# Optimization experiments

Hardware: AMD Instinct MI355X
Metric: run time of the kernel (lower is better)

The kernel has to match this reference:

```python
import jax, jax.numpy as jnp
import numpy as np

SEQ_LEN, N_FEAT, EMB = 512, 8, 64
HID = 2 * EMB  # 128
BATCH = 512


def _lstm_layer(x, Wih, Whh, bih, bhh):
    """Single-layer LSTM, batch_first x: [B,T,F]. PyTorch gate order i,f,g,o.
    Returns (outputs [B,T,H], final hidden [B,H])."""
    B = x.shape[0]
    H = Whh.shape[1]
    # precompute input projections for all timesteps: [B,T,4H]
    xp = jnp.einsum('btf,gf->btg', x, Wih) + bih + bhh

    def step(carry, xt):
        h, c = carry
        gates = xt + h @ Whh.T  # [B,4H]
        i, f, g, o = jnp.split(gates, 4, axis=-1)
        i = jax.nn.sigmoid(i)
        f = jax.nn.sigmoid(f)
        g = jnp.tanh(g)
        o = jax.nn.sigmoid(o)
        c = f * c + i * g
        h = o * jnp.tanh(c)
        return (h, c), h

    h0 = jnp.zeros((B, H), dtype=x.dtype)
    c0 = jnp.zeros((B, H), dtype=x.dtype)
    (hT, _), hs = jax.lax.scan(step, (h0, c0), xp.transpose(1, 0, 2))
    return hs.transpose(1, 0, 2), hT


def setup_inputs() -> dict:
    key = jax.random.key(0)
    ks = jax.random.split(key, 13)
    inp = {"x": jax.random.normal(ks[0], (BATCH, SEQ_LEN, N_FEAT), dtype=jnp.float32)}

    def mk(k, shape, fan):
        s = 1.0 / np.sqrt(fan)
        return jax.random.uniform(k, shape, dtype=jnp.float32, minval=-s, maxval=s)

    # layer 1: in=N_FEAT, hid=HID
    inp["Wih1"] = mk(ks[1], (4 * HID, N_FEAT), HID)
    inp["Whh1"] = mk(ks[2], (4 * HID, HID), HID)
    inp["bih1"] = mk(ks[3], (4 * HID,), HID)
    inp["bhh1"] = mk(ks[4], (4 * HID,), HID)
    # layer 2: in=HID, hid=HID
    inp["Wih2"] = mk(ks[5], (4 * HID, HID), HID)
    inp["Whh2"] = mk(ks[6], (4 * HID, HID), HID)
    inp["bih2"] = mk(ks[7], (4 * HID,), HID)
    inp["bhh2"] = mk(ks[8], (4 * HID,), HID)
    # layer 3: in=HID, hid=EMB
    inp["Wih3"] = mk(ks[9], (4 * EMB, HID), EMB)
    inp["Whh3"] = mk(ks[10], (4 * EMB, EMB), EMB)
    inp["bih3"] = mk(ks[11], (4 * EMB,), EMB)
    inp["bhh3"] = mk(ks[12], (4 * EMB,), EMB)
    return inp


def reference(x, Wih1, Whh1, bih1, bhh1, Wih2, Whh2, bih2, bhh2, Wih3, Whh3, bih3, bhh3):
    B = x.shape[0]
    x = x.reshape(B, SEQ_LEN, N_FEAT)
    x, _ = _lstm_layer(x, Wih1, Whh1, bih1, bhh1)
    x, _ = _lstm_layer(x, Wih2, Whh2, bih2, bhh2)
    _, hT = _lstm_layer(x, Wih3, Whh3, bih3, bhh3)
    return hT  # [B, EMB]
```

## Files before the change

### kernel.cpp

```cpp
#include <hip/hip_runtime.h>


#define DEVI __device__ __forceinline__

typedef _Float16 h8 __attribute__((ext_vector_type(8)));
typedef float f4 __attribute__((ext_vector_type(4)));

static constexpr int T_ = 512, TC_ = 16, NC_ = T_ / TC_;

DEVI float sigmoidf_(float x) {
    return __builtin_amdgcn_rcpf(1.f + __builtin_amdgcn_exp2f(x * -1.44269504f));
}
DEVI float tanhf_(float x) {
    return 2.f * __builtin_amdgcn_rcpf(1.f + __builtin_amdgcn_exp2f(x * -2.88539008f)) - 1.f;
}

DEVI h8 cvt8(const float* p) {
    const float4 a = *reinterpret_cast<const float4*>(p);
    const float4 b = *reinterpret_cast<const float4*>(p + 4);
    return h8{(_Float16)a.x, (_Float16)a.y, (_Float16)a.z, (_Float16)a.w,
              (_Float16)b.x, (_Float16)b.y, (_Float16)b.z, (_Float16)b.w};
}

DEVI void lds_barrier() {
    asm volatile("s_waitcnt lgkmcnt(0)\n\ts_barrier" ::: "memory");
}

template <int LAYER>
DEVI void stage(int tile, char* smem, const float* x, const _Float16* Oin,
                const float* Wih, const float* Whh, const float* bih,
                const float* bhh, _Float16* Oout, float* out,
                int* flag_in, int* flag_out) {
    constexpr int H = (LAYER == 3) ? 64 : 128;
    constexpr int KT_H = H / 32;
    constexpr int KT_X = (LAYER == 1) ? 1 : 4;
    constexpr int HP = H + 8;
    constexpr int NWAVE = (LAYER == 3) ? 4 : 8;

    const int tid  = threadIdx.x;
    const int lane = tid & 63;
    const int wv   = tid >> 6;
    const int lr   = lane & 15;
    const int lk   = lane >> 4;
    const int b0   = tile * 16;
    const bool active = (wv < NWAVE);
    const int jcol = (wv & (NWAVE - 1)) * 16 + lr;

    _Float16 (*h_lds)[16][HP] = (_Float16 (*)[16][HP])smem;

    h8 wbh[4][KT_H], wbx[4][KT_X];
    float bias[4];
    if (active) {
#pragma unroll
        for (int q = 0; q < 4; q++) {
#pragma unroll
            for (int kt = 0; kt < KT_H; kt++)
                wbh[q][kt] = cvt8(Whh + (size_t)(q * H + jcol) * H + kt * 32 + lk * 8);
            if constexpr (LAYER == 1) {
                wbx[q][0] = (lk == 0) ? cvt8(Wih + (size_t)(q * H + jcol) * 8) : h8{};
            } else {
#pragma unroll
                for (int kt = 0; kt < KT_X; kt++)
                    wbx[q][kt] = cvt8(Wih + (size_t)(q * H + jcol) * 128 + kt * 32 + lk * 8);
            }
            bias[q] = bih[q * H + jcol] + bhh[q * H + jcol];
        }
    }

    float c[4] = {0.f, 0.f, 0.f, 0.f};

    for (int i = tid; i < 2 * 16 * HP; i += 512) ((_Float16*)smem)[i] = (_Float16)0;
    __syncthreads();

    auto load_x = [&](int t, h8* xa) {
        if constexpr (LAYER == 1) {
            xa[0] = (lk == 0) ? cvt8(x + ((size_t)(b0 + lr) * T_ + t) * 8) : h8{};
        } else {
#pragma unroll
            for (int kt = 0; kt < KT_X; kt++)
                xa[kt] = *reinterpret_cast<const h8*>(
                    Oin + ((size_t)(b0 + lr) * T_ + t) * 128 + kt * 32 + lk * 8);
        }
    };

    auto xmfma = [&](const h8* xv, f4* ax) {
#pragma unroll
        for (int q = 0; q < 4; q++) ax[q] = f4{bias[q], bias[q], bias[q], bias[q]};
#pragma unroll
        for (int kt = 0; kt < KT_X; kt++)
#pragma unroll
            for (int q = 0; q < 4; q++)
                ax[q] = __builtin_amdgcn_mfma_f32_16x16x32_f16(xv[kt], wbx[q][kt], ax[q], 0, 0, 0);
    };

    h8 xa[KT_X], xn[KT_X];
    f4 accx[4];

    for (int ch = 0; ch < NC_; ch++) {
        if constexpr (LAYER > 1) {
            if (tid == 0) {
                while (__hip_atomic_load(flag_in, __ATOMIC_RELAXED,
                                         __HIP_MEMORY_SCOPE_AGENT) < ch + 1)
                    __builtin_amdgcn_s_sleep(2);
                __threadfence();
            }
            __syncthreads();
        }
        if (active) {
            load_x(ch * TC_, xa);
            xmfma(xa, accx);
        }

        for (int tt = 0; tt < TC_; tt++) {
            const int t = ch * TC_ + tt;
            const int cur = t & 1;
            if (active) {
                h8 ha[KT_H];
#pragma unroll
                for (int kt = 0; kt < KT_H; kt++)
                    ha[kt] = *reinterpret_cast<const h8*>(&h_lds[cur][lr][kt * 32 + lk * 8]);

                f4 acc[4];
#pragma unroll
                for (int q = 0; q < 4; q++) acc[q] = accx[q];

#pragma unroll
                for (int kt = 0; kt < KT_H; kt++)
#pragma unroll
                    for (int q = 0; q < 4; q++)
                        acc[q] = __builtin_amdgcn_mfma_f32_16x16x32_f16(ha[kt], wbh[q][kt], acc[q], 0, 0, 0);

                if (tt + 1 < TC_) load_x(t + 1, xn);

#pragma unroll
                for (int i = 0; i < 4; i++) {
                    const float gi = sigmoidf_(acc[0][i]);
                    const float gf = sigmoidf_(acc[1][i]);
                    const float gg = tanhf_(acc[2][i]);
                    const float go = sigmoidf_(acc[3][i]);
                    c[i] = gf * c[i] + gi * gg;
                    const float h = go * tanhf_(c[i]);
                    const int row = lk * 4 + i;
                    h_lds[cur ^ 1][row][jcol] = (_Float16)h;
                    if constexpr (LAYER < 3) {
                        Oout[((size_t)(b0 + row) * T_ + t) * 128 + jcol] = (_Float16)h;
                    } else {
                        if (t == T_ - 1) out[(size_t)(b0 + row) * 64 + jcol] = h;
                    }
                }

                if (tt + 1 < TC_) {
                    xmfma(xn, accx);
#pragma unroll
                    for (int kt = 0; kt < KT_X; kt++) xa[kt] = xn[kt];
                }
            }
            lds_barrier();
        }

        if constexpr (LAYER < 3) {
            asm volatile("s_waitcnt vmcnt(0)" ::: "memory");
            __syncthreads();
            if (tid == 0) {
                __threadfence();
                __hip_atomic_store(flag_out, ch + 1, __ATOMIC_RELAXED,
                                   __HIP_MEMORY_SCOPE_AGENT);
            }
        }
    }
}

__global__ __launch_bounds__(512, 1)
void mega_k(const float* __restrict__ x,
            const float* __restrict__ Wih1, const float* __restrict__ Whh1,
            const float* __restrict__ bih1, const float* __restrict__ bhh1,
            const float* __restrict__ Wih2, const float* __restrict__ Whh2,
            const float* __restrict__ bih2, const float* __restrict__ bhh2,
            const float* __restrict__ Wih3, const float* __restrict__ Whh3,
            const float* __restrict__ bih3, const float* __restrict__ bhh3,
            _Float16* __restrict__ O1, _Float16* __restrict__ O2,
            float* __restrict__ out, int* __restrict__ flags) {
    extern __shared__ char smem[];
    const int bid = blockIdx.x;
    if (bid < 32) {
        stage<1>(bid, smem, x, nullptr, Wih1, Whh1, bih1, bhh1, O1, nullptr,
                 nullptr, flags + bid);
    } else if (bid < 64) {
        stage<2>(bid - 32, smem, nullptr, O1, Wih2, Whh2, bih2, bhh2, O2, nullptr,
                 flags + (bid - 32), flags + 32 + (bid - 32));
    } else {
        stage<3>(bid - 64, smem, nullptr, O2, Wih3, Whh3, bih3, bhh3, nullptr, out,
                 flags + 32 + (bid - 64), nullptr);
    }
}

__global__ void zero_flags_k(int* flags) {
    if (threadIdx.x < 64)
        __hip_atomic_store(flags + threadIdx.x, 0, __ATOMIC_RELAXED,
                           __HIP_MEMORY_SCOPE_AGENT);
}

extern "C" void kernel_launch(void* const* d_in, const int* in_sizes, int n_in,
                              void* d_out, int out_size, void* d_ws, size_t ws_size,
                              hipStream_t stream) {
    const float* x    = (const float*)d_in[0];
    float* out = (float*)d_out;

    char* ws = (char*)d_ws;
    _Float16* O1 = (_Float16*)ws;
    _Float16* O2 = (_Float16*)(ws + (size_t)67108864);
    int* flags   = (int*)(ws + (size_t)134217728);
    (void)ws_size; (void)in_sizes; (void)n_in; (void)out_size;

    zero_flags_k<<<1, 64, 0, stream>>>(flags);
    mega_k<<<96, 512, 8704, stream>>>(
        x,
        (const float*)d_in[1], (const float*)d_in[2], (const float*)d_in[3], (const float*)d_in[4],
        (const float*)d_in[5], (const float*)d_in[6], (const float*)d_in[7], (const float*)d_in[8],
        (const float*)d_in[9], (const float*)d_in[10], (const float*)d_in[11], (const float*)d_in[12],
        O1, O2, out, flags);
}
```

Measured before the change: 806.2 us.

## Split input projection onto separate producer waves via LDS double buffer

Each block grows to 1024 threads: waves 0-7 run the recurrent h@Whh MFMA and gate math, and waves 8-15 compute the input projection for the next timestep. The projection is written into a double-buffered fp32 LDS array that the recurrent waves read. This takes the Wih MFMAs and input loads off the serial recurrence's critical path and lowers per-wave register pressure. The cost is more LDS (about 90KB), a larger block, and an extra LDS round trip each step.

```diff
diff --git a/kernel.cpp b/kernel.cpp
--- a/kernel.cpp
+++ b/kernel.cpp
@@ -6,7 +6,7 @@
 typedef _Float16 h8 __attribute__((ext_vector_type(8)));
 typedef float f4 __attribute__((ext_vector_type(4)));
 
-static constexpr int T_ = 512, TC_ = 16, NC_ = T_ / TC_;
+static constexpr int T_ = 512, TC_ = 16, NC_ = T_ / TC_, XGP = 20;
 
 DEVI float sigmoidf_(float x) {
     return __builtin_amdgcn_rcpf(1.f + __builtin_amdgcn_exp2f(x * -1.44269504f));
@@ -14,89 +14,102 @@
 DEVI float tanhf_(float x) {
     return 2.f * __builtin_amdgcn_rcpf(1.f + __builtin_amdgcn_exp2f(x * -2.88539008f)) - 1.f;
 }
-
 DEVI h8 cvt8(const float* p) {
     const float4 a = *reinterpret_cast<const float4*>(p);
     const float4 b = *reinterpret_cast<const float4*>(p + 4);
     return h8{(_Float16)a.x, (_Float16)a.y, (_Float16)a.z, (_Float16)a.w,
               (_Float16)b.x, (_Float16)b.y, (_Float16)b.z, (_Float16)b.w};
 }
-
 DEVI void lds_barrier() {
     asm volatile("s_waitcnt lgkmcnt(0)\n\ts_barrier" ::: "memory");
 }
 
 template <int LAYER>
 DEVI void stage(int tile, char* smem, const float* x, const _Float16* Oin,
-                const float* Wih, const float* Whh, const float* bih,
-                const float* bhh, _Float16* Oout, float* out,
+                _Float16* Oout, const float* Wih, const float* Whh,
+                const float* bih, const float* bhh, float* out,
                 int* flag_in, int* flag_out) {
     constexpr int H = (LAYER == 3) ? 64 : 128;
+    constexpr int G = 4 * H;
     constexpr int KT_H = H / 32;
     constexpr int KT_X = (LAYER == 1) ? 1 : 4;
     constexpr int HP = H + 8;
-    constexpr int NWAVE = (LAYER == 3) ? 4 : 8;
-
-    const int tid  = threadIdx.x;
-    const int lane = tid & 63;
-    const int wv   = tid >> 6;
-    const int lr   = lane & 15;
-    const int lk   = lane >> 4;
-    const int b0   = tile * 16;
-    const bool active = (wv < NWAVE);
-    const int jcol = (wv & (NWAVE - 1)) * 16 + lr;
-
-    _Float16 (*h_lds)[16][HP] = (_Float16 (*)[16][HP])smem;
-
-    h8 wbh[4][KT_H], wbx[4][KT_X];
-    float bias[4];
-    if (active) {
-#pragma unroll
-        for (int q = 0; q < 4; q++) {
+    constexpr int NWR = H / 16;
+    constexpr int PNT = G / 128;
+
+    const int tid = threadIdx.x, lane = tid & 63, wv = tid >> 6;
+    const int lr = lane & 15, lk = lane >> 4;
+    const int b0 = tile * 16;
+    const bool isrec = (wv < 8);
+    const bool recact = (wv < NWR);
+
+    float* xg = (float*)smem;
+    _Float16 (*h_lds)[16][HP] =
+        (_Float16 (*)[16][HP])(smem + (size_t)2 * G * XGP * 4);
+
+    h8 wreg[16];
+    f4 acc[4];
+    h8 opf[4];
+    float pbias[4];
+    float c[4] = {0.f, 0.f, 0.f, 0.f};
+    int jcol = 0, gc0 = 0;
+
+    if (isrec) {
+        jcol = (wv & (NWR - 1)) * 16 + lr;
+        if (recact) {
 #pragma unroll
             for (int kt = 0; kt < KT_H; kt++)
-                wbh[q][kt] = cvt8(Whh + (size_t)(q * H + jcol) * H + kt * 32 + lk * 8);
+#pragma unroll
+                for (int q = 0; q < 4; q++)
+                    wreg[kt * 4 + q] = cvt8(Whh + (size_t)(q * H + jcol) * H + kt * 32 + lk * 8);
+        }
+    } else {
+        const int pw = wv - 8;
+        gc0 = pw * (16 * PNT);
+#pragma unroll
+        for (int nt = 0; nt < PNT; nt++) {
+            const int gcol = gc0 + nt * 16 + lr;
+            pbias[nt] = bih[gcol] + bhh[gcol];
             if constexpr (LAYER == 1) {
-                wbx[q][0] = (lk == 0) ? cvt8(Wih + (size_t)(q * H + jcol) * 8) : h8{};
+                wreg[nt] = (lk == 0) ? cvt8(Wih + (size_t)gcol * 8) : h8{};
             } else {
 #pragma unroll
                 for (int kt = 0; kt < KT_X; kt++)
-                    wbx[q][kt] = cvt8(Wih + (size_t)(q * H + jcol) * 128 + kt * 32 + lk * 8);
-            }
-            bias[q] = bih[q * H + jcol] + bhh[q * H + jcol];
+                    wreg[nt * KT_X + kt] = cvt8(Wih + (size_t)gcol * 128 + kt * 32 + lk * 8);
+            }
         }
     }
 
-    float c[4] = {0.f, 0.f, 0.f, 0.f};
-
-    for (int i = tid; i < 2 * 16 * HP; i += 512) ((_Float16*)smem)[i] = (_Float16)0;
+    for (int i = tid; i < 2 * 16 * HP; i += 1024)
+        ((_Float16*)(smem + (size_t)2 * G * XGP * 4))[i] = (_Float16)0;
     __syncthreads();
 
-    auto load_x = [&](int t, h8* xa) {
+    auto proj_step = [&](int t) {
         if constexpr (LAYER == 1) {
-            xa[0] = (lk == 0) ? cvt8(x + ((size_t)(b0 + lr) * T_ + t) * 8) : h8{};
+            opf[0] = (lk == 0) ? cvt8(x + ((size_t)(b0 + lr) * T_ + t) * 8) : h8{};
         } else {
 #pragma unroll
             for (int kt = 0; kt < KT_X; kt++)
-                xa[kt] = *reinterpret_cast<const h8*>(
+                opf[kt] = *reinterpret_cast<const h8*>(
                     Oin + ((size_t)(b0 + lr) * T_ + t) * 128 + kt * 32 + lk * 8);
         }
+#pragma unroll
+        for (int nt = 0; nt < PNT; nt++)
+            acc[nt] = f4{pbias[nt], pbias[nt], pbias[nt], pbias[nt]};
+#pragma unroll
+        for (int kt = 0; kt < KT_X; kt++)
+#pragma unroll
+            for (int nt = 0; nt < PNT; nt++)
+                acc[nt] = __builtin_amdgcn_mfma_f32_16x16x32_f16(opf[kt], wreg[nt * KT_X + kt],
+                                                                 acc[nt], 0, 0, 0);
+        float* dst = xg + (size_t)(t & 1) * G * XGP;
+#pragma unroll
+        for (int nt = 0; nt < PNT; nt++)
+            *reinterpret_cast<f4*>(dst + (gc0 + nt * 16 + lr) * XGP + lk * 4) = acc[nt];
     };
 
-    auto xmfma = [&](const h8* xv, f4* ax) {
-#pragma unroll
-        for (int q = 0; q < 4; q++) ax[q] = f4{bias[q], bias[q], bias[q], bias[q]};
-#pragma unroll
-        for (int kt = 0; kt < KT_X; kt++)
-#pragma unroll
-            for (int q = 0; q < 4; q++)
-                ax[q] = __builtin_amdgcn_mfma_f32_16x16x32_f16(xv[kt], wbx[q][kt], ax[q], 0, 0, 0);
-    };
-
-    h8 xa[KT_X], xn[KT_X];
-    f4 accx[4];
-
     for (int ch = 0; ch < NC_; ch++) {
+        const int t0 = ch * TC_;
         if constexpr (LAYER > 1) {
             if (tid == 0) {
                 while (__hip_atomic_load(flag_in, __ATOMIC_RELAXED,
@@ -104,64 +117,58 @@
                     __builtin_amdgcn_s_sleep(2);
                 __threadfence();
             }
-            __syncthreads();
-        }
-        if (active) {
-            load_x(ch * TC_, xa);
-            xmfma(xa, accx);
-        }
+        }
+        __syncthreads();
+        if (!isrec) proj_step(t0);
+        lds_barrier();
 
         for (int tt = 0; tt < TC_; tt++) {
-            const int t = ch * TC_ + tt;
+            const int t = t0 + tt;
             const int cur = t & 1;
-            if (active) {
-                h8 ha[KT_H];
-#pragma unroll
-                for (int kt = 0; kt < KT_H; kt++)
-                    ha[kt] = *reinterpret_cast<const h8*>(&h_lds[cur][lr][kt * 32 + lk * 8]);
-
-                f4 acc[4];
-#pragma unroll
-                for (int q = 0; q < 4; q++) acc[q] = accx[q];
-
-#pragma unroll
-                for (int kt = 0; kt < KT_H; kt++)
+            if (isrec) {
+                if (recact) {
+                    const float* src = xg + (size_t)cur * G * XGP;
 #pragma unroll
                     for (int q = 0; q < 4; q++)
-                        acc[q] = __builtin_amdgcn_mfma_f32_16x16x32_f16(ha[kt], wbh[q][kt], acc[q], 0, 0, 0);
-
-                if (tt + 1 < TC_) load_x(t + 1, xn);
-
-#pragma unroll
-                for (int i = 0; i < 4; i++) {
-                    const float gi = sigmoidf_(acc[0][i]);
-                    const float gf = sigmoidf_(acc[1][i]);
-                    const float gg = tanhf_(acc[2][i]);
-                    const float go = sigmoidf_(acc[3][i]);
-                    c[i] = gf * c[i] + gi * gg;
-                    const float h = go * tanhf_(c[i]);
-                    const int row = lk * 4 + i;
-                    h_lds[cur ^ 1][row][jcol] = (_Float16)h;
-                    if constexpr (LAYER < 3) {
-                        Oout[((size_t)(b0 + row) * T_ + t) * 128 + jcol] = (_Float16)h;
-                    } else {
-                        if (t == T_ - 1) out[(size_t)(b0 + row) * 64 + jcol] = h;
+                        acc[q] = *reinterpret_cast<const f4*>(src + (q * H + jcol) * XGP + lk * 4);
+#pragma unroll
+                    for (int kt = 0; kt < KT_H; kt++)
+                        opf[kt] = *reinterpret_cast<const h8*>(&h_lds[cur][lr][kt * 32 + lk * 8]);
+#pragma unroll
+                    for (int kt = 0; kt < KT_H; kt++)
+#pragma unroll
+                        for (int q = 0; q < 4; q++)
+                            acc[q] = __builtin_amdgcn_mfma_f32_16x16x32_f16(opf[kt], wreg[kt * 4 + q],
+                                                                            acc[q], 0, 0, 0);
+#pragma unroll
+                    for (int i = 0; i < 4; i++) {
+                        const float gi = sigmoidf_(acc[0][i]);
+                        const float gf = sigmoidf_(acc[1][i]);
+                        const float gg = tanhf_(acc[2][i]);
+                        const float go = sigmoidf_(acc[3][i]);
+                        c[i] = gf * c[i] + gi * gg;
+                        const float h = go * tanhf_(c[i]);
+                        const int row = lk * 4 + i;
+                        h_lds[cur ^ 1][row][jcol] = (_Float16)h;
+                        if constexpr (LAYER < 3) {
+                            Oout[((size_t)(b0 + row) * T_ + t) * 128 + jcol] = (_Float16)h;
+                        } else {
+                            if (t == T_ - 1) out[(size_t)(b0 + row) * 64 + jcol] = h;
+                        }
                     }
                 }
-
-                if (tt + 1 < TC_) {
-                    xmfma(xn, accx);
-#pragma unroll
-                    for (int kt = 0; kt < KT_X; kt++) xa[kt] = xn[kt];
-                }
+            } else {
+                if (tt + 1 < TC_) proj_step(t + 1);
             }
             lds_barrier();
         }
 
         if constexpr (LAYER < 3) {
             asm volatile("s_waitcnt vmcnt(0)" ::: "memory");
-            __syncthreads();
-            if (tid == 0) {
+        }
+        __syncthreads();
+        if (tid == 0) {
+            if constexpr (LAYER < 3) {
                 __threadfence();
                 __hip_atomic_store(flag_out, ch + 1, __ATOMIC_RELAXED,
                                    __HIP_MEMORY_SCOPE_AGENT);
@@ -170,7 +177,7 @@
     }
 }
 
-__global__ __launch_bounds__(512, 1)
+__global__ __launch_bounds__(1024, 4)
 void mega_k(const float* __restrict__ x,
             const float* __restrict__ Wih1, const float* __restrict__ Whh1,
             const float* __restrict__ bih1, const float* __restrict__ bhh1,
@@ -183,13 +190,13 @@
     extern __shared__ char smem[];
     const int bid = blockIdx.x;
     if (bid < 32) {
-        stage<1>(bid, smem, x, nullptr, Wih1, Whh1, bih1, bhh1, O1, nullptr,
+        stage<1>(bid, smem, x, nullptr, O1, Wih1, Whh1, bih1, bhh1, nullptr,
                  nullptr, flags + bid);
     } else if (bid < 64) {
-        stage<2>(bid - 32, smem, nullptr, O1, Wih2, Whh2, bih2, bhh2, O2, nullptr,
+        stage<2>(bid - 32, smem, nullptr, O1, O2, Wih2, Whh2, bih2, bhh2, nullptr,
                  flags + (bid - 32), flags + 32 + (bid - 32));
     } else {
-        stage<3>(bid - 64, smem, nullptr, O2, Wih3, Whh3, bih3, bhh3, nullptr, out,
+        stage<3>(bid - 64, smem, nullptr, O2, nullptr, Wih3, Whh3, bih3, bhh3, out,
                  flags + 32 + (bid - 64), nullptr);
     }
 }
@@ -203,7 +210,7 @@
 extern "C" void kernel_launch(void* const* d_in, const int* in_sizes, int n_in,
                               void* d_out, int out_size, void* d_ws, size_t ws_size,
                               hipStream_t stream) {
-    const float* x    = (const float*)d_in[0];
+    const float* x = (const float*)d_in[0];
     float* out = (float*)d_out;
 
     char* ws = (char*)d_ws;
@@ -213,7 +220,7 @@
     (void)ws_size; (void)in_sizes; (void)n_in; (void)out_size;
 
     zero_flags_k<<<1, 64, 0, stream>>>(flags);
-    mega_k<<<96, 512, 8704, stream>>>(
+    mega_k<<<96, 1024, 90624, stream>>>(
         x,
         (const float*)d_in[1], (const float*)d_in[2], (const float*)d_in[3], (const float*)d_in[4],
         (const float*)d_in[5], (const float*)d_in[6], (const float*)d_in[7], (const float*)d_in[8],
```

New measurement: 1.142 ms. 1.42x slower.

## Split layer-2 input projection into separate stage with ring buffers

Applied to the files above, without the earlier changes.

Adds a fourth pipeline stage of 32 blocks that computes layer 2's input projection (Wih2·h1 + bias) ahead of time. The results go into a two-slot ring buffer with producer and consumer flags, so the layer-2 recurrence only does the Whh matmul on its serial critical path. Layer 1 now writes its outputs into a small ring buffer instead of a full tensor. The step loops are also unrolled by two, and the exponentials are issued before the reciprocals. The cost is 128 resident blocks, more flag traffic, backpressure stalls on layer 1, and fp16 rounding of the precomputed gate inputs.

```diff
diff --git a/kernel.cpp b/kernel.cpp
--- a/kernel.cpp
+++ b/kernel.cpp
@@ -3,17 +3,14 @@
 
 #define DEVI __device__ __forceinline__
 
+typedef _Float16 h4 __attribute__((ext_vector_type(4)));
 typedef _Float16 h8 __attribute__((ext_vector_type(8)));
 typedef float f4 __attribute__((ext_vector_type(4)));
 
-static constexpr int T_ = 512, TC_ = 16, NC_ = T_ / TC_;
-
-DEVI float sigmoidf_(float x) {
-    return __builtin_amdgcn_rcpf(1.f + __builtin_amdgcn_exp2f(x * -1.44269504f));
-}
-DEVI float tanhf_(float x) {
-    return 2.f * __builtin_amdgcn_rcpf(1.f + __builtin_amdgcn_exp2f(x * -2.88539008f)) - 1.f;
-}
+static constexpr int T_ = 512, TC_ = 16, NC_ = T_ / TC_, RC_ = 2;
+
+DEVI float rcpf_(float x) { return __builtin_amdgcn_rcpf(x); }
+DEVI float exp2f_(float x) { return __builtin_amdgcn_exp2f(x); }
 
 DEVI h8 cvt8(const float* p) {
     const float4 a = *reinterpret_cast<const float4*>(p);
@@ -25,149 +22,293 @@
 DEVI void lds_barrier() {
     asm volatile("s_waitcnt lgkmcnt(0)\n\ts_barrier" ::: "memory");
 }
-
-template <int LAYER>
-DEVI void stage(int tile, char* smem, const float* x, const _Float16* Oin,
-                const float* Wih, const float* Whh, const float* bih,
-                const float* bhh, _Float16* Oout, float* out,
-                int* flag_in, int* flag_out) {
-    constexpr int H = (LAYER == 3) ? 64 : 128;
-    constexpr int KT_H = H / 32;
-    constexpr int KT_X = (LAYER == 1) ? 1 : 4;
-    constexpr int HP = H + 8;
-    constexpr int NWAVE = (LAYER == 3) ? 4 : 8;
-
-    const int tid  = threadIdx.x;
-    const int lane = tid & 63;
-    const int wv   = tid >> 6;
-    const int lr   = lane & 15;
-    const int lk   = lane >> 4;
-    const int b0   = tile * 16;
-    const bool active = (wv < NWAVE);
-    const int jcol = (wv & (NWAVE - 1)) * 16 + lr;
-
+DEVI int ld_flag(int* f) {
+    return __hip_atomic_load(f, __ATOMIC_RELAXED, __HIP_MEMORY_SCOPE_AGENT);
+}
+DEVI void st_flag(int* f, int v) {
+    __hip_atomic_store(f, v, __ATOMIC_RELAXED, __HIP_MEMORY_SCOPE_AGENT);
+}
+
+#define POINTWISE_PROLOG(ACC)                                                   \
+    float e0[4], e1[4], e2[4], e3[4];                                           \
+    _Pragma("unroll") for (int i = 0; i < 4; i++) {                             \
+        e0[i] = exp2f_(ACC[0][i] * -1.44269504f);                               \
+        e1[i] = exp2f_(ACC[1][i] * -1.44269504f);                               \
+        e2[i] = exp2f_(ACC[2][i] * -2.88539008f);                               \
+        e3[i] = exp2f_(ACC[3][i] * -1.44269504f); }
+
+#define POINTWISE_CELL(i, C, HVAR)                                              \
+    const float gi = rcpf_(1.f + e0[i]), gf = rcpf_(1.f + e1[i]);               \
+    const float gg = 2.f * rcpf_(1.f + e2[i]) - 1.f, go = rcpf_(1.f + e3[i]);   \
+    C[i] = gf * C[i] + gi * gg;                                                 \
+    const float HVAR = go * (2.f * rcpf_(1.f + exp2f_(C[i] * -2.88539008f)) - 1.f);
+
+DEVI void stage_L1(int tile, char* smem, const float* x, const float* Wih,
+                   const float* Whh, const float* bih, const float* bhh,
+                   _Float16* o1, int* c1, int* p1) {
+    constexpr int H = 128, KT_H = 4, HP = H + 8;
+    const int tid = threadIdx.x, lane = tid & 63, wv = tid >> 6;
+    const int lr = lane & 15, lk = lane >> 4;
+    const int b0 = tile * 16;
+    const int jcol = wv * 16 + lr;
+    _Float16 (*h_lds)[16][HP] = (_Float16 (*)[16][HP])smem;
+
+    h8 wbh[4][KT_H], wbx[4];
+    float bias[4];
+#pragma unroll
+    for (int q = 0; q < 4; q++) {
+#pragma unroll
+        for (int kt = 0; kt < KT_H; kt++)
+            wbh[q][kt] = cvt8(Whh + (size_t)(q * H + jcol) * H + kt * 32 + lk * 8);
+        wbx[q] = (lk == 0) ? cvt8(Wih + (size_t)(q * H + jcol) * 8) : h8{};
+        bias[q] = bih[q * H + jcol] + bhh[q * H + jcol];
+    }
+    float c[4] = {0.f, 0.f, 0.f, 0.f};
+    for (int i = tid; i < 2 * 16 * HP; i += 512) ((_Float16*)smem)[i] = (_Float16)0;
+    __syncthreads();
+
+    auto load_x = [&](int t, h8& xa) {
+        xa = (lk == 0) ? cvt8(x + ((size_t)(b0 + lr) * T_ + t) * 8) : h8{};
+    };
+    h8 xa, xb;
+
+#define L1_STEP(TT, CUR, XS) {                                                  \
+    const int tt = (TT);                                                        \
+    h8 ha[KT_H];                                                                \
+    _Pragma("unroll") for (int kt = 0; kt < KT_H; kt++)                         \
+        ha[kt] = *reinterpret_cast<const h8*>(&h_lds[CUR][lr][kt * 32 + lk * 8]); \
+    f4 acc[4];                                                                  \
+    _Pragma("unroll") for (int q = 0; q < 4; q++)                               \
+        acc[q] = f4{bias[q], bias[q], bias[q], bias[q]};                        \
+    _Pragma("unroll") for (int q = 0; q < 4; q++)                               \
+        acc[q] = __builtin_amdgcn_mfma_f32_16x16x32_f16(XS, wbx[q], acc[q], 0, 0, 0); \
+    _Pragma("unroll") for (int kt = 0; kt < KT_H; kt++)                         \
+        _Pragma("unroll") for (int q = 0; q < 4; q++)                           \
+            acc[q] = __builtin_amdgcn_mfma_f32_16x16x32_f16(ha[kt], wbh[q][kt], acc[q], 0, 0, 0); \
+    if (tt + 2 < TC_) load_x(t0 + tt + 2, XS);                                  \
+    POINTWISE_PROLOG(acc)                                                       \
+    _Pragma("unroll") for (int i = 0; i < 4; i++) {                             \
+        POINTWISE_CELL(i, c, h)                                                 \
+        const int row = lk * 4 + i;                                             \
+        h_lds[(CUR) ^ 1][row][jcol] = (_Float16)h;                              \
+        o1[(((size_t)(tile * RC_ + slot) * TC_ + tt) * 16 + row) * 128 + jcol] = (_Float16)h; } }
+
+    for (int ch = 0; ch < NC_; ch++) {
+        const int slot = ch & (RC_ - 1);
+        if (tid == 0) {
+            while (ld_flag(c1) < ch - (RC_ - 1)) __builtin_amdgcn_s_sleep(8);
+        }
+        __syncthreads();
+        const int t0 = ch * TC_;
+        load_x(t0, xa); load_x(t0 + 1, xb);
+        for (int tb = 0; tb < TC_ / 2; tb++) {
+            L1_STEP(2 * tb, 0, xa) lds_barrier();
+            L1_STEP(2 * tb + 1, 1, xb) lds_barrier();
+        }
+        asm volatile("s_waitcnt vmcnt(0)" ::: "memory");
+        __syncthreads();
+        if (tid == 0) { __threadfence(); st_flag(p1, ch + 1); }
+    }
+#undef L1_STEP
+}
+
+DEVI void stage_P2(int tile, const _Float16* o1, _Float16* xp, const float* Wih,
+                   const float* bih, const float* bhh,
+                   int* p1, int* c1, int* cx, int* px) {
+    constexpr int H = 128;
+    const int tid = threadIdx.x, lane = tid & 63, wv = tid >> 6;
+    const int lr = lane & 15, lk = lane >> 4;
+    const int jcol = wv * 16 + lr;
+
+    h8 wbx[4][4];
+    float pbias[4];
+#pragma unroll
+    for (int q = 0; q < 4; q++) {
+#pragma unroll
+        for (int kt = 0; kt < 4; kt++)
+            wbx[q][kt] = cvt8(Wih + (size_t)(q * H + jcol) * 128 + kt * 32 + lk * 8);
+        pbias[q] = bih[q * H + jcol] + bhh[q * H + jcol];
+    }
+
+    for (int ch = 0; ch < NC_; ch++) {
+        const int slot = ch & (RC_ - 1);
+        if (tid == 0) {
+            while (ld_flag(p1) < ch + 1) __builtin_amdgcn_s_sleep(8);
+            while (ld_flag(cx) < ch - (RC_ - 1)) __builtin_amdgcn_s_sleep(8);
+            __threadfence();
+        }
+        __syncthreads();
+        const size_t ib = (size_t)(tile * RC_ + slot) * TC_ * 2048;
+        const size_t ob = (size_t)(tile * RC_ + slot) * TC_ * 8192;
+#pragma unroll 4
+        for (int t = 0; t < TC_; t++) {
+            h8 af[4];
+#pragma unroll
+            for (int kt = 0; kt < 4; kt++)
+                af[kt] = *reinterpret_cast<const h8*>(o1 + ib + (size_t)t * 2048 + lr * 128 + kt * 32 + lk * 8);
+            f4 acc[4];
+#pragma unroll
+            for (int q = 0; q < 4; q++) acc[q] = f4{pbias[q], pbias[q], pbias[q], pbias[q]};
+#pragma unroll
+            for (int kt = 0; kt < 4; kt++)
+#pragma unroll
+                for (int q = 0; q < 4; q++)
+                    acc[q] = __builtin_amdgcn_mfma_f32_16x16x32_f16(af[kt], wbx[q][kt], acc[q], 0, 0, 0);
+#pragma unroll
+            for (int q = 0; q < 4; q++) {
+                const h4 o = h4{(_Float16)acc[q][0], (_Float16)acc[q][1],
+                                (_Float16)acc[q][2], (_Float16)acc[q][3]};
+                *reinterpret_cast<h4*>(xp + ob + (size_t)t * 8192 + (wv * 4 + q) * 256 + lane * 4) = o;
+            }
+        }
+        asm volatile("s_waitcnt vmcnt(0)" ::: "memory");
+        __syncthreads();
+        if (tid == 0) { __threadfence(); st_flag(px, ch + 1); st_flag(c1, ch + 1); }
+    }
+}
+
+DEVI void stage_L2(int tile, char* smem, const _Float16* xp, _Float16* O2,
+                   const float* Whh, int* px, int* cx, int* p2) {
+    constexpr int H = 128, KT_H = 4, HP = H + 8;
+    const int tid = threadIdx.x, lane = tid & 63, wv = tid >> 6;
+    const int lr = lane & 15, lk = lane >> 4;
+    const int b0 = tile * 16;
+    const int jcol = wv * 16 + lr;
+    _Float16 (*h_lds)[16][HP] = (_Float16 (*)[16][HP])smem;
+
+    h8 wbh[4][KT_H];
+#pragma unroll
+    for (int q = 0; q < 4; q++)
+#pragma unroll
+        for (int kt = 0; kt < KT_H; kt++)
+            wbh[q][kt] = cvt8(Whh + (size_t)(q * H + jcol) * H + kt * 32 + lk * 8);
+
+    float c[4] = {0.f, 0.f, 0.f, 0.f};
+    for (int i = tid; i < 2 * 16 * HP; i += 512) ((_Float16*)smem)[i] = (_Float16)0;
+    __syncthreads();
+
+    h4 xqa[4], xqb[4];
+
+#define LOAD_XP(SLOT, TTL, DST) {                                               \
+    const size_t base = ((size_t)(tile * RC_ + (SLOT)) * TC_ + (TTL)) * 8192 + wv * 1024 + lane * 4; \
+    _Pragma("unroll") for (int q = 0; q < 4; q++)                               \
+        DST[q] = *reinterpret_cast<const h4*>(xp + base + q * 256); }
+
+#define L2_STEP(TT, CUR, XQ) {                                                  \
+    const int tt = (TT); const int t = t0 + tt;                                 \
+    h8 ha[KT_H];                                                                \
+    _Pragma("unroll") for (int kt = 0; kt < KT_H; kt++)                         \
+        ha[kt] = *reinterpret_cast<const h8*>(&h_lds[CUR][lr][kt * 32 + lk * 8]); \
+    f4 acc[4];                                                                  \
+    _Pragma("unroll") for (int q = 0; q < 4; q++)                               \
+        acc[q] = f4{(float)XQ[q][0], (float)XQ[q][1], (float)XQ[q][2], (float)XQ[q][3]}; \
+    _Pragma("unroll") for (int kt = 0; kt < KT_H; kt++)                         \
+        _Pragma("unroll") for (int q = 0; q < 4; q++)                           \
+            acc[q] = __builtin_amdgcn_mfma_f32_16x16x32_f16(ha[kt], wbh[q][kt], acc[q], 0, 0, 0); \
+    if (tt + 2 < TC_) LOAD_XP(slot, tt + 2, XQ)                                 \
+    POINTWISE_PROLOG(acc)                                                       \
+    _Pragma("unroll") for (int i = 0; i < 4; i++) {                             \
+        POINTWISE_CELL(i, c, h)                                                 \
+        const int row = lk * 4 + i;                                             \
+        h_lds[(CUR) ^ 1][row][jcol] = (_Float16)h;                              \
+        O2[((size_t)(b0 + row) * T_ + t) * 128 + jcol] = (_Float16)h; } }
+
+    for (int ch = 0; ch < NC_; ch++) {
+        const int slot = ch & (RC_ - 1);
+        if (tid == 0) {
+            while (ld_flag(px) < ch + 1) __builtin_amdgcn_s_sleep(8);
+            __threadfence();
+        }
+        __syncthreads();
+        const int t0 = ch * TC_;
+        LOAD_XP(slot, 0, xqa)
+        LOAD_XP(slot, 1, xqb)
+        for (int tb = 0; tb < TC_ / 2; tb++) {
+            L2_STEP(2 * tb, 0, xqa) lds_barrier();
+            L2_STEP(2 * tb + 1, 1, xqb) lds_barrier();
+        }
+        asm volatile("s_waitcnt vmcnt(0)" ::: "memory");
+        __syncthreads();
+        if (tid == 0) { __threadfence(); st_flag(p2, ch + 1); st_flag(cx, ch + 1); }
+    }
+#undef L2_STEP
+#undef LOAD_XP
+}
+
+DEVI void stage_L3(int tile, char* smem, const _Float16* O2, const float* Wih,
+                   const float* Whh, const float* bih, const float* bhh,
+                   float* out, int* p2) {
+    constexpr int H = 64, KT_H = 2, KT_X = 4, HP = H + 8;
+    const int tid = threadIdx.x, lane = tid & 63, wv = tid >> 6;
+    const int lr = lane & 15, lk = lane >> 4;
+    const int b0 = tile * 16;
+    const bool act = (wv < 4);
+    const int jcol = (wv & 3) * 16 + lr;
     _Float16 (*h_lds)[16][HP] = (_Float16 (*)[16][HP])smem;
 
     h8 wbh[4][KT_H], wbx[4][KT_X];
     float bias[4];
-    if (active) {
+    if (act) {
 #pragma unroll
         for (int q = 0; q < 4; q++) {
 #pragma unroll
             for (int kt = 0; kt < KT_H; kt++)
                 wbh[q][kt] = cvt8(Whh + (size_t)(q * H + jcol) * H + kt * 32 + lk * 8);
-            if constexpr (LAYER == 1) {
-                wbx[q][0] = (lk == 0) ? cvt8(Wih + (size_t)(q * H + jcol) * 8) : h8{};
-            } else {
-#pragma unroll
-                for (int kt = 0; kt < KT_X; kt++)
-                    wbx[q][kt] = cvt8(Wih + (size_t)(q * H + jcol) * 128 + kt * 32 + lk * 8);
-            }
+#pragma unroll
+            for (int kt = 0; kt < KT_X; kt++)
+                wbx[q][kt] = cvt8(Wih + (size_t)(q * H + jcol) * 128 + kt * 32 + lk * 8);
             bias[q] = bih[q * H + jcol] + bhh[q * H + jcol];
         }
     }
-
     float c[4] = {0.f, 0.f, 0.f, 0.f};
-
     for (int i = tid; i < 2 * 16 * HP; i += 512) ((_Float16*)smem)[i] = (_Float16)0;
     __syncthreads();
 
     auto load_x = [&](int t, h8* xa) {
-        if constexpr (LAYER == 1) {
-            xa[0] = (lk == 0) ? cvt8(x + ((size_t)(b0 + lr) * T_ + t) * 8) : h8{};
-        } else {
-#pragma unroll
-            for (int kt = 0; kt < KT_X; kt++)
-                xa[kt] = *reinterpret_cast<const h8*>(
-                    Oin + ((size_t)(b0 + lr) * T_ + t) * 128 + kt * 32 + lk * 8);
-        }
+#pragma unroll
+        for (int kt = 0; kt < KT_X; kt++)
+            xa[kt] = *reinterpret_cast<const h8*>(
+                O2 + ((size_t)(b0 + lr) * T_ + t) * 128 + kt * 32 + lk * 8);
     };
-
-    auto xmfma = [&](const h8* xv, f4* ax) {
-#pragma unroll
-        for (int q = 0; q < 4; q++) ax[q] = f4{bias[q], bias[q], bias[q], bias[q]};
-#pragma unroll
-        for (int kt = 0; kt < KT_X; kt++)
-#pragma unroll
-            for (int q = 0; q < 4; q++)
-                ax[q] = __builtin_amdgcn_mfma_f32_16x16x32_f16(xv[kt], wbx[q][kt], ax[q], 0, 0, 0);
-    };
-
-    h8 xa[KT_X], xn[KT_X];
-    f4 accx[4];
+    h8 xa[KT_X], xb[KT_X];
+
+#define L3_STEP(TT, CUR, XS) {                                                  \
+    const int tt = (TT); const int t = t0 + tt;                                 \
+    if (act) {                                                                  \
+        h8 ha[KT_H];                                                            \
+        _Pragma("unroll") for (int kt = 0; kt < KT_H; kt++)                     \
+            ha[kt] = *reinterpret_cast<const h8*>(&h_lds[CUR][lr][kt * 32 + lk * 8]); \
+        f4 acc[4];                                                              \
+        _Pragma("unroll") for (int q = 0; q < 4; q++)                           \
+            acc[q] = f4{bias[q], bias[q], bias[q], bias[q]};                    \
+        _Pragma("unroll") for (int kt = 0; kt < KT_X; kt++)                     \
+            _Pragma("unroll") for (int q = 0; q < 4; q++)                       \
+                acc[q] = __builtin_amdgcn_mfma_f32_16x16x32_f16(XS[kt], wbx[q][kt], acc[q], 0, 0, 0); \
+        _Pragma("unroll") for (int kt = 0; kt < KT_H; kt++)                     \
+            _Pragma("unroll") for (int q = 0; q < 4; q++)                       \
+                acc[q] = __builtin_amdgcn_mfma_f32_16x16x32_f16(ha[kt], wbh[q][kt], acc[q], 0, 0, 0); \
+        if (tt + 2 < TC_) load_x(t + 2, XS);                                    \
+        POINTWISE_PROLOG(acc)                                                   \
+        _Pragma("unroll") for (int i = 0; i < 4; i++) {                         \
+            POINTWISE_CELL(i, c, h)                                             \
+            const int row = lk * 4 + i;                                         \
+            h_lds[(CUR) ^ 1][row][jcol] = (_Float16)h;                          \
+            if (t == T_ - 1) out[(size_t)(b0 + row) * 64 + jcol] = h; } } }
 
     for (int ch = 0; ch < NC_; ch++) {
-        if constexpr (LAYER > 1) {
-            if (tid == 0) {
-                while (__hip_atomic_load(flag_in, __ATOMIC_RELAXED,
-                                         __HIP_MEMORY_SCOPE_AGENT) < ch + 1)
-                    __builtin_amdgcn_s_sleep(2);
-                __threadfence();
-            }
-            __syncthreads();
-        }
-        if (active) {
-            load_x(ch * TC_, xa);
-            xmfma(xa, accx);
-        }
-
-        for (int tt = 0; tt < TC_; tt++) {
-            const int t = ch * TC_ + tt;
-            const int cur = t & 1;
-            if (active) {
-                h8 ha[KT_H];
-#pragma unroll
-                for (int kt = 0; kt < KT_H; kt++)
-                    ha[kt] = *reinterpret_cast<const h8*>(&h_lds[cur][lr][kt * 32 + lk * 8]);
-
-                f4 acc[4];
-#pragma unroll
-                for (int q = 0; q < 4; q++) acc[q] = accx[q];
-
-#pragma unroll
-                for (int kt = 0; kt < KT_H; kt++)
-#pragma unroll
-                    for (int q = 0; q < 4; q++)
-                        acc[q] = __builtin_amdgcn_mfma_f32_16x16x32_f16(ha[kt], wbh[q][kt], acc[q], 0, 0, 0);
-
-                if (tt + 1 < TC_) load_x(t + 1, xn);
-
-#pragma unroll
-                for (int i = 0; i < 4; i++) {
-                    const float gi = sigmoidf_(acc[0][i]);
-                    const float gf = sigmoidf_(acc[1][i]);
-                    const float gg = tanhf_(acc[2][i]);
-                    const float go = sigmoidf_(acc[3][i]);
-                    c[i] = gf * c[i] + gi * gg;
-                    const float h = go * tanhf_(c[i]);
-                    const int row = lk * 4 + i;
-                    h_lds[cur ^ 1][row][jcol] = (_Float16)h;
-                    if constexpr (LAYER < 3) {
-                        Oout[((size_t)(b0 + row) * T_ + t) * 128 + jcol] = (_Float16)h;
-                    } else {
-                        if (t == T_ - 1) out[(size_t)(b0 + row) * 64 + jcol] = h;
-                    }
-                }
-
-                if (tt + 1 < TC_) {
-                    xmfma(xn, accx);
-#pragma unroll
-                    for (int kt = 0; kt < KT_X; kt++) xa[kt] = xn[kt];
-                }
-            }
-            lds_barrier();
-        }
-
-        if constexpr (LAYER < 3) {
-            asm volatile("s_waitcnt vmcnt(0)" ::: "memory");
-            __syncthreads();
-            if (tid == 0) {
-                __threadfence();
-                __hip_atomic_store(flag_out, ch + 1, __ATOMIC_RELAXED,
-                                   __HIP_MEMORY_SCOPE_AGENT);
-            }
-        }
-    }
+        if (tid == 0) {
+            while (ld_flag(p2) < ch + 1) __builtin_amdgcn_s_sleep(8);
+            __threadfence();
+        }
+        __syncthreads();
+        const int t0 = ch * TC_;
+        if (act) { load_x(t0, xa); load_x(t0 + 1, xb); }
+        for (int tb = 0; tb < TC_ / 2; tb++) {
+            L3_STEP(2 * tb, 0, xa) lds_barrier();
+            L3_STEP(2 * tb + 1, 1, xb) lds_barrier();
+        }
+    }
+#undef L3_STEP
 }
 
 __global__ __launch_bounds__(512, 1)
@@ -178,24 +319,32 @@
             const float* __restrict__ bih2, const float* __restrict__ bhh2,
             const float* __restrict__ Wih3, const float* __restrict__ Whh3,
             const float* __restrict__ bih3, const float* __restrict__ bhh3,
-            _Float16* __restrict__ O1, _Float16* __restrict__ O2,
-            float* __restrict__ out, int* __restrict__ flags) {
+            _Float16* __restrict__ o1ring, _Float16* __restrict__ xpring,
+            _Float16* __restrict__ O2, float* __restrict__ out,
+            int* __restrict__ flags) {
     extern __shared__ char smem[];
     const int bid = blockIdx.x;
+    int* p1 = flags;
+    int* c1 = flags + 32;
+    int* px = flags + 64;
+    int* cx = flags + 96;
+    int* p2 = flags + 128;
     if (bid < 32) {
-        stage<1>(bid, smem, x, nullptr, Wih1, Whh1, bih1, bhh1, O1, nullptr,
-                 nullptr, flags + bid);
+        stage_L1(bid, smem, x, Wih1, Whh1, bih1, bhh1, o1ring, c1 + bid, p1 + bid);
     } else if (bid < 64) {
-        stage<2>(bid - 32, smem, nullptr, O1, Wih2, Whh2, bih2, bhh2, O2, nullptr,
-                 flags + (bid - 32), flags + 32 + (bid - 32));
+        const int t = bid - 32;
+        stage_P2(t, o1ring, xpring, Wih2, bih2, bhh2, p1 + t, c1 + t, cx + t, px + t);
+    } else if (bid < 96) {
+        const int t = bid - 64;
+        stage_L2(t, smem, xpring, O2, Whh2, px + t, cx + t, p2 + t);
     } else {
-        stage<3>(bid - 64, smem, nullptr, O2, Wih3, Whh3, bih3, bhh3, nullptr, out,
-                 flags + 32 + (bid - 64), nullptr);
+        const int t = bid - 96;
+        stage_L3(t, smem, O2, Wih3, Whh3, bih3, bhh3, out, p2 + t);
     }
 }
 
 __global__ void zero_flags_k(int* flags) {
-    if (threadIdx.x < 64)
+    if (threadIdx.x < 160)
         __hip_atomic_store(flags + threadIdx.x, 0, __ATOMIC_RELAXED,
                            __HIP_MEMORY_SCOPE_AGENT);
 }
@@ -203,20 +352,21 @@
 extern "C" void kernel_launch(void* const* d_in, const int* in_sizes, int n_in,
                               void* d_out, int out_size, void* d_ws, size_t ws_size,
                               hipStream_t stream) {
-    const float* x    = (const float*)d_in[0];
+    const float* x = (const float*)d_in[0];
     float* out = (float*)d_out;
 
     char* ws = (char*)d_ws;
-    _Float16* O1 = (_Float16*)ws;
-    _Float16* O2 = (_Float16*)(ws + (size_t)67108864);
-    int* flags   = (int*)(ws + (size_t)134217728);
+    _Float16* o1ring = (_Float16*)ws;
+    _Float16* xpring = (_Float16*)(ws + (size_t)4194304);
+    _Float16* O2     = (_Float16*)(ws + (size_t)20971520);
+    int* flags       = (int*)(ws + (size_t)88080384);
     (void)ws_size; (void)in_sizes; (void)n_in; (void)out_size;
 
-    zero_flags_k<<<1, 64, 0, stream>>>(flags);
-    mega_k<<<96, 512, 8704, stream>>>(
+    zero_flags_k<<<1, 192, 0, stream>>>(flags);
+    mega_k<<<128, 512, 8704, stream>>>(
         x,
         (const float*)d_in[1], (const float*)d_in[2], (const float*)d_in[3], (const float*)d_in[4],
         (const float*)d_in[5], (const float*)d_in[6], (const float*)d_in[7], (const float*)d_in[8],
         (const float*)d_in[9], (const float*)d_in[10], (const float*)d_in[11], (const float*)d_in[12],
-        O1, O2, out, flags);
-}
+        o1ring, xpring, O2, out, flags);
+}
```

Measured after the change: 711.4 us. -11.8%, faster.
